# Kernel optimization log

Measured on AMD Instinct MI355X. Metric: run time of the kernel, lower is better.

Reference implementation:

```python
import jax, jax.numpy as jnp
import numpy as np

B, S, D, H = 4, 2048, 1024, 16
DH = D // H  # 64


def setup_inputs() -> dict:
    key = jax.random.key(0)
    ks = jax.random.split(key, 7)
    scale = 1.0 / np.sqrt(DH)
    return {
        "sequences": jax.random.normal(ks[0], (B, S, D), dtype=jnp.float32),
        # torch Linear weights: [out, in] per head -> stacked [H, DH, DH]
        "Wq": jax.random.uniform(ks[1], (H, DH, DH), jnp.float32, -scale, scale),
        "bq": jax.random.uniform(ks[2], (H, DH), jnp.float32, -scale, scale),
        "Wk": jax.random.uniform(ks[3], (H, DH, DH), jnp.float32, -scale, scale),
        "bk": jax.random.uniform(ks[4], (H, DH), jnp.float32, -scale, scale),
        "Wv": jax.random.uniform(ks[5], (H, DH, DH), jnp.float32, -scale, scale),
        "bv": jax.random.uniform(ks[6], (H, DH), jnp.float32, -scale, scale),
    }


def reference(sequences, Wq, bq, Wk, bk, Wv, bv):
    # split d into heads: [B, S, H, DH]
    x = sequences.reshape(B, S, H, DH)
    # per-head Linear: y = x @ W.T + b
    q = jnp.einsum("bshd,hed->bshe", x, Wq) + bq
    k = jnp.einsum("bshd,hed->bshe", x, Wk) + bk
    v = jnp.einsum("bshd,hed->bshe", x, Wv) + bv
    # scaled dot-product attention per head
    scores = jnp.einsum("bshd,bthd->bhst", q, k) / jnp.sqrt(jnp.float32(DH))
    attn = jax.nn.softmax(scores, axis=-1)
    out = jnp.einsum("bhst,bthd->bshd", attn, v)
    # hstack heads back to [B, S, D]
    return out.reshape(B, S, D)
```

## Files before the change

kernel.cpp:

```cpp
#include <hip/hip_runtime.h>
#include <hip/hip_bf16.h>


typedef unsigned short u16;
typedef unsigned int   u32;
typedef float  f32x4   __attribute__((ext_vector_type(4)));
typedef float  f32x16  __attribute__((ext_vector_type(16)));
typedef __bf16 bf16x4  __attribute__((ext_vector_type(4)));
typedef __bf16 bf16x8  __attribute__((ext_vector_type(8)));

#define NB 4
#define SS 2048
#define DDIM 1024
#define NH 16
#define DH 64

static __device__ __forceinline__ float fexp2(float x) {
#if __has_builtin(__builtin_amdgcn_exp2f)
    return __builtin_amdgcn_exp2f(x);
#else
    return exp2f(x);
#endif
}
static __device__ __forceinline__ bf16x4 cvt4(f32x4 v) {
    return __builtin_convertvector(v, bf16x4);
}
static __device__ __forceinline__ bf16x8 cvt8(f32x4 lo, f32x4 hi) {
    return __builtin_shufflevector(cvt4(lo), cvt4(hi), 0, 1, 2, 3, 4, 5, 6, 7);
}

#define WST 72

__global__ __launch_bounds__(256) void qkv_kernel(
        const float* __restrict__ x,
        const float* __restrict__ Wq, const float* __restrict__ bq,
        const float* __restrict__ Wk, const float* __restrict__ bk,
        const float* __restrict__ Wv, const float* __restrict__ bv,
        u16* __restrict__ Qw, u16* __restrict__ Kw, u16* __restrict__ Vt) {
    __shared__ __align__(16) u16 W_lds[3 * DH * WST];

    const int tid  = threadIdx.x;
    const int w    = tid >> 6;
    const int lane = tid & 63;
    const int quad = lane >> 4;
    const int c    = lane & 15;
    const int bid  = blockIdx.x;
    const int bh   = bid & 63;
    const int s0   = (bid >> 6) * 256;
    const int b    = bh >> 4, h = bh & 15;

    {
        const float* Wsrc[3] = {Wq + h*DH*DH, Wk + h*DH*DH, Wv + h*DH*DH};
        #pragma unroll
        for (int j = 0; j < 6; ++j) {
            const int m = j >> 1;
            const int chunk = ((j & 1) << 8) + tid;
            const float* src = Wsrc[m] + chunk * 8;
            f32x4 lo = *(const f32x4*)src;
            f32x4 hi = *(const f32x4*)(src + 4);
            const int row = chunk >> 3, c8 = chunk & 7;
            *(bf16x8*)&W_lds[(m*DH + row) * WST + c8*8] = cvt8(lo, hi);
        }
    }
    __syncthreads();

    bf16x8 wf[3][4][2];
    #pragma unroll
    for (int m = 0; m < 3; ++m)
        #pragma unroll
        for (int mt = 0; mt < 4; ++mt)
            #pragma unroll
            for (int kh = 0; kh < 2; ++kh)
                wf[m][mt][kh] = *(const bf16x8*)&W_lds[(m*DH + mt*16 + c) * WST + kh*32 + quad*8];

    f32x4 biasQK[2][4];
    float biasV[4];
    #pragma unroll
    for (int mt = 0; mt < 4; ++mt) {
        biasQK[0][mt] = *(const f32x4*)(bq + h*DH + mt*16 + quad*4);
        biasQK[1][mt] = *(const f32x4*)(bk + h*DH + mt*16 + quad*4);
        biasV[mt] = bv[h*DH + mt*16 + c];
    }

    const size_t qkbase = (size_t)bh * SS * DH;
    const size_t vtbase = (size_t)bh * DH * SS;

    #pragma unroll 1
    for (int g = 0; g < 4; ++g) {
        const int sb = s0 + w*64 + g*16;
        const float* xr = x + ((size_t)(b * SS + sb + c)) * DDIM + h * DH;
        bf16x8 xb[2];
        #pragma unroll
        for (int kh = 0; kh < 2; ++kh) {
            f32x4 lo = *(const f32x4*)(xr + kh*32 + quad*8);
            f32x4 hi = *(const f32x4*)(xr + kh*32 + quad*8 + 4);
            xb[kh] = cvt8(lo, hi);
        }

        const int srow = sb + c;
        const int tq = srow & 31;
        const int sK = (srow & ~31) | (tq & 3)
                     | (((tq >> 3) & 1) << 2)
                     | (((tq >> 2) & 1) << 3)
                     | (((tq >> 4) & 1) << 4);

        #pragma unroll
        for (int m = 0; m < 2; ++m) {
            const float scale = (m == 0) ? 0.18033688f : 1.0f;
            u16* base = (m == 0 ? Qw : Kw) + qkbase + (size_t)(m == 0 ? srow : sK) * DH;
            #pragma unroll
            for (int mt = 0; mt < 4; ++mt) {
                f32x4 acc = {0.f, 0.f, 0.f, 0.f};
                acc = __builtin_amdgcn_mfma_f32_16x16x32_bf16(wf[m][mt][0], xb[0], acc, 0, 0, 0);
                acc = __builtin_amdgcn_mfma_f32_16x16x32_bf16(wf[m][mt][1], xb[1], acc, 0, 0, 0);
                f32x4 v = (acc + biasQK[m][mt]) * scale;
                *(bf16x4*)(base + mt*16 + quad*4) = cvt4(v);
            }
        }
        #pragma unroll
        for (int nt = 0; nt < 4; ++nt) {
            f32x4 acc = {0.f, 0.f, 0.f, 0.f};
            acc = __builtin_amdgcn_mfma_f32_16x16x32_bf16(xb[0], wf[2][nt][0], acc, 0, 0, 0);
            acc = __builtin_amdgcn_mfma_f32_16x16x32_bf16(xb[1], wf[2][nt][1], acc, 0, 0, 0);
            f32x4 v = acc + biasV[nt];
            u16* dst = Vt + vtbase + (size_t)(nt*16 + c) * SS + sb + quad*4;
            *(bf16x4*)dst = cvt4(v);
        }
    }
}

#define KT 64
#define KST 72
#define VST 72

#define Z16 {0.f,0.f,0.f,0.f,0.f,0.f,0.f,0.f,0.f,0.f,0.f,0.f,0.f,0.f,0.f,0.f}

#define GROUP(g) do {                                                          \
        bf16x8 ka0 = *(const bf16x8*)&Kl[((g)*32 + l31) * KST +  0 + hi*8];    \
        bf16x8 ka1 = *(const bf16x8*)&Kl[((g)*32 + l31) * KST + 16 + hi*8];    \
        bf16x8 ka2 = *(const bf16x8*)&Kl[((g)*32 + l31) * KST + 32 + hi*8];    \
        bf16x8 ka3 = *(const bf16x8*)&Kl[((g)*32 + l31) * KST + 48 + hi*8];    \
        bf16x8 vf00 = *(const bf16x8*)&Vl[( 0 + l31) * VST + (g)*32 +  0 + hi*8]; \
        bf16x8 vf01 = *(const bf16x8*)&Vl[( 0 + l31) * VST + (g)*32 + 16 + hi*8]; \
        bf16x8 vf10 = *(const bf16x8*)&Vl[(32 + l31) * VST + (g)*32 +  0 + hi*8]; \
        bf16x8 vf11 = *(const bf16x8*)&Vl[(32 + l31) * VST + (g)*32 + 16 + hi*8]; \
        __builtin_amdgcn_s_setprio(1);                                         \
        f32x16 s = Z16;                                                        \
        s = __builtin_amdgcn_mfma_f32_32x32x16_bf16(ka0, qf[0], s, 0,0,0);     \
        s = __builtin_amdgcn_mfma_f32_32x32x16_bf16(ka1, qf[1], s, 0,0,0);     \
        s = __builtin_amdgcn_mfma_f32_32x32x16_bf16(ka2, qf[2], s, 0,0,0);     \
        s = __builtin_amdgcn_mfma_f32_32x32x16_bf16(ka3, qf[3], s, 0,0,0);     \
        _Pragma("unroll")                                                      \
        for (int r = 0; r < 16; ++r) s[r] = fexp2(s[r]);                       \
        lp += (((s[0]+s[1])+(s[2]+s[3])) + ((s[4]+s[5])+(s[6]+s[7])))          \
            + (((s[8]+s[9])+(s[10]+s[11])) + ((s[12]+s[13])+(s[14]+s[15])));   \
        bf16x8 pf0 = cvt8((f32x4){s[0],s[1],s[2],s[3]},                        \
                          (f32x4){s[4],s[5],s[6],s[7]});                       \
        bf16x8 pf1 = cvt8((f32x4){s[8],s[9],s[10],s[11]},                      \
                          (f32x4){s[12],s[13],s[14],s[15]});                   \
        o0 = __builtin_amdgcn_mfma_f32_32x32x16_bf16(vf00, pf0, o0, 0,0,0);    \
        o0 = __builtin_amdgcn_mfma_f32_32x32x16_bf16(vf01, pf1, o0, 0,0,0);    \
        o1 = __builtin_amdgcn_mfma_f32_32x32x16_bf16(vf10, pf0, o1, 0,0,0);    \
        o1 = __builtin_amdgcn_mfma_f32_32x32x16_bf16(vf11, pf1, o1, 0,0,0);    \
        __builtin_amdgcn_s_setprio(0);                                         \
    } while (0)

__global__ __launch_bounds__(256, 2) void attn_kernel(
        const u16* __restrict__ Qw, const u16* __restrict__ Kw,
        const u16* __restrict__ Vt, float* __restrict__ out) {
    __shared__ __align__(16) u16 K_lds[2][KT * KST];
    __shared__ __align__(16) u16 V_lds[2][DH * VST];

    const int tid  = threadIdx.x;
    const int w    = tid >> 6;
    const int lane = tid & 63;
    const int l31  = lane & 31;
    const int hi   = lane >> 5;
    const int bid  = blockIdx.x;
    const int bh   = bid & 63;
    const int q0   = (bid >> 6) * 128;
    const int qw   = q0 + w * 32;

    const u16* Qb = Qw + (size_t)bh * SS * DH;
    const u16* Kb = Kw + (size_t)bh * SS * DH;
    const u16* Vb = Vt + (size_t)bh * DH * SS;

    bf16x8 qf[4];
    {
        const u16* qrow = Qb + (size_t)(qw + l31) * DH;
        #pragma unroll
        for (int m = 0; m < 4; ++m)
            qf[m] = *(const bf16x8*)(qrow + m*16 + hi*8);
    }

    f32x16 o0 = Z16, o1 = Z16;
    float lp = 0.f;

    const int strow = tid >> 2;
    const int stcol = (tid & 3) * 16;
    const int kofs  = strow * KST + stcol;
    const int vofs  = strow * VST + stcol;

    uint4 kr0 = *(const uint4*)(Kb + (size_t)strow * DH + stcol);
    uint4 kr1 = *(const uint4*)(Kb + (size_t)strow * DH + stcol + 8);
    uint4 vr0 = *(const uint4*)(Vb + (size_t)strow * SS + stcol);
    uint4 vr1 = *(const uint4*)(Vb + (size_t)strow * SS + stcol + 8);

    #pragma unroll 1
    for (int t0 = 0; t0 < SS; t0 += KT) {
        const int bsel = (t0 >> 6) & 1;
        u16* Kl = K_lds[bsel];
        u16* Vl = V_lds[bsel];
        *(uint4*)&Kl[kofs]     = kr0;
        *(uint4*)&Kl[kofs + 8] = kr1;
        *(uint4*)&Vl[vofs]     = vr0;
        *(uint4*)&Vl[vofs + 8] = vr1;
        __syncthreads();
        int tn = t0 + KT; if (tn >= SS) tn = 0;
        kr0 = *(const uint4*)(Kb + (size_t)(tn + strow) * DH + stcol);
        kr1 = *(const uint4*)(Kb + (size_t)(tn + strow) * DH + stcol + 8);
        vr0 = *(const uint4*)(Vb + (size_t)strow * SS + tn + stcol);
        vr1 = *(const uint4*)(Vb + (size_t)strow * SS + tn + stcol + 8);

        GROUP(0);
        GROUP(1);
    }

    const int b = bh >> 4, h = bh & 15;
    const float lw = lp + __shfl_xor(lp, 32, 64);
    const float inv = 1.0f / lw;
    const int token = qw + l31;
    float* orow = out + ((size_t)b * SS + token) * DDIM + h * DH;
    #pragma unroll
    for (int rq = 0; rq < 4; ++rq) {
        f32x4 v0 = {o0[4*rq+0], o0[4*rq+1], o0[4*rq+2], o0[4*rq+3]};
        f32x4 v1 = {o1[4*rq+0], o1[4*rq+1], o1[4*rq+2], o1[4*rq+3]};
        v0 = v0 * inv;
        v1 = v1 * inv;
        *(f32x4*)(orow +      8*rq + 4*hi) = v0;
        *(f32x4*)(orow + 32 + 8*rq + 4*hi) = v1;
    }
}

extern "C" void kernel_launch(void* const* d_in, const int* in_sizes, int n_in,
                              void* d_out, int out_size, void* d_ws, size_t ws_size,
                              hipStream_t stream) {
    const float* x  = (const float*)d_in[0];
    const float* Wq = (const float*)d_in[1];
    const float* bq = (const float*)d_in[2];
    const float* Wk = (const float*)d_in[3];
    const float* bk = (const float*)d_in[4];
    const float* Wv = (const float*)d_in[5];
    const float* bv = (const float*)d_in[6];

    u16* Qw = (u16*)d_ws;
    u16* Kw = Qw + (size_t)NB * NH * SS * DH;
    u16* Vt = Kw + (size_t)NB * NH * SS * DH;

    qkv_kernel<<<64 * (SS / 256), 256, 0, stream>>>(
        x, Wq, bq, Wk, bk, Wv, bv, Qw, Kw, Vt);
    attn_kernel<<<64 * (SS / 128), 256, 0, stream>>>(Qw, Kw, Vt, (float*)d_out);
}
```

Baseline: 186.0 us.

## Software-pipeline QK^T of the next group with exp/PV of the previous

```diff
diff --git a/kernel.cpp b/kernel.cpp
--- a/kernel.cpp
+++ b/kernel.cpp
@@ -135,21 +135,26 @@
 
 #define Z16 {0.f,0.f,0.f,0.f,0.f,0.f,0.f,0.f,0.f,0.f,0.f,0.f,0.f,0.f,0.f,0.f}
 
-#define GROUP(g) do {                                                          \
-        bf16x8 ka0 = *(const bf16x8*)&Kl[((g)*32 + l31) * KST +  0 + hi*8];    \
-        bf16x8 ka1 = *(const bf16x8*)&Kl[((g)*32 + l31) * KST + 16 + hi*8];    \
-        bf16x8 ka2 = *(const bf16x8*)&Kl[((g)*32 + l31) * KST + 32 + hi*8];    \
-        bf16x8 ka3 = *(const bf16x8*)&Kl[((g)*32 + l31) * KST + 48 + hi*8];    \
-        bf16x8 vf00 = *(const bf16x8*)&Vl[( 0 + l31) * VST + (g)*32 +  0 + hi*8]; \
-        bf16x8 vf01 = *(const bf16x8*)&Vl[( 0 + l31) * VST + (g)*32 + 16 + hi*8]; \
-        bf16x8 vf10 = *(const bf16x8*)&Vl[(32 + l31) * VST + (g)*32 +  0 + hi*8]; \
-        bf16x8 vf11 = *(const bf16x8*)&Vl[(32 + l31) * VST + (g)*32 + 16 + hi*8]; \
-        __builtin_amdgcn_s_setprio(1);                                         \
-        f32x16 s = Z16;                                                        \
-        s = __builtin_amdgcn_mfma_f32_32x32x16_bf16(ka0, qf[0], s, 0,0,0);     \
-        s = __builtin_amdgcn_mfma_f32_32x32x16_bf16(ka1, qf[1], s, 0,0,0);     \
-        s = __builtin_amdgcn_mfma_f32_32x32x16_bf16(ka2, qf[2], s, 0,0,0);     \
-        s = __builtin_amdgcn_mfma_f32_32x32x16_bf16(ka3, qf[3], s, 0,0,0);     \
+#define QKG(Kp, g, sdst) do {                                                  \
+        bf16x8 ka0 = *(const bf16x8*)&Kp[((g)*32 + l31) * KST +  0 + hi*8];    \
+        bf16x8 ka1 = *(const bf16x8*)&Kp[((g)*32 + l31) * KST + 16 + hi*8];    \
+        bf16x8 ka2 = *(const bf16x8*)&Kp[((g)*32 + l31) * KST + 32 + hi*8];    \
+        bf16x8 ka3 = *(const bf16x8*)&Kp[((g)*32 + l31) * KST + 48 + hi*8];    \
+        sdst = (f32x16)Z16;                                                    \
+        sdst = __builtin_amdgcn_mfma_f32_32x32x16_bf16(ka0, qf[0], sdst, 0,0,0); \
+        sdst = __builtin_amdgcn_mfma_f32_32x32x16_bf16(ka1, qf[1], sdst, 0,0,0); \
+        sdst = __builtin_amdgcn_mfma_f32_32x32x16_bf16(ka2, qf[2], sdst, 0,0,0); \
+        sdst = __builtin_amdgcn_mfma_f32_32x32x16_bf16(ka3, qf[3], sdst, 0,0,0); \
+    } while (0)
+
+#define VFR(Vp, g, vf) do {                                                    \
+        vf[0] = *(const bf16x8*)&Vp[( 0 + l31) * VST + (g)*32 +  0 + hi*8];    \
+        vf[1] = *(const bf16x8*)&Vp[( 0 + l31) * VST + (g)*32 + 16 + hi*8];    \
+        vf[2] = *(const bf16x8*)&Vp[(32 + l31) * VST + (g)*32 +  0 + hi*8];    \
+        vf[3] = *(const bf16x8*)&Vp[(32 + l31) * VST + (g)*32 + 16 + hi*8];    \
+    } while (0)
+
+#define FIN(s, vf) do {                                                        \
         _Pragma("unroll")                                                      \
         for (int r = 0; r < 16; ++r) s[r] = fexp2(s[r]);                       \
         lp += (((s[0]+s[1])+(s[2]+s[3])) + ((s[4]+s[5])+(s[6]+s[7])))          \
@@ -158,11 +163,10 @@
                           (f32x4){s[4],s[5],s[6],s[7]});                       \
         bf16x8 pf1 = cvt8((f32x4){s[8],s[9],s[10],s[11]},                      \
                           (f32x4){s[12],s[13],s[14],s[15]});                   \
-        o0 = __builtin_amdgcn_mfma_f32_32x32x16_bf16(vf00, pf0, o0, 0,0,0);    \
-        o0 = __builtin_amdgcn_mfma_f32_32x32x16_bf16(vf01, pf1, o0, 0,0,0);    \
-        o1 = __builtin_amdgcn_mfma_f32_32x32x16_bf16(vf10, pf0, o1, 0,0,0);    \
-        o1 = __builtin_amdgcn_mfma_f32_32x32x16_bf16(vf11, pf1, o1, 0,0,0);    \
-        __builtin_amdgcn_s_setprio(0);                                         \
+        o0 = __builtin_amdgcn_mfma_f32_32x32x16_bf16(vf[0], pf0, o0, 0,0,0);   \
+        o0 = __builtin_amdgcn_mfma_f32_32x32x16_bf16(vf[1], pf1, o0, 0,0,0);   \
+        o1 = __builtin_amdgcn_mfma_f32_32x32x16_bf16(vf[2], pf0, o1, 0,0,0);   \
+        o1 = __builtin_amdgcn_mfma_f32_32x32x16_bf16(vf[3], pf1, o1, 0,0,0);   \
     } while (0)
 
 __global__ __launch_bounds__(256, 2) void attn_kernel(
@@ -206,24 +210,56 @@
     uint4 vr0 = *(const uint4*)(Vb + (size_t)strow * SS + stcol);
     uint4 vr1 = *(const uint4*)(Vb + (size_t)strow * SS + stcol + 8);
 
+    *(uint4*)&K_lds[0][kofs]     = kr0;
+    *(uint4*)&K_lds[0][kofs + 8] = kr1;
+    *(uint4*)&V_lds[0][vofs]     = vr0;
+    *(uint4*)&V_lds[0][vofs + 8] = vr1;
+    __syncthreads();
+    kr0 = *(const uint4*)(Kb + (size_t)(KT + strow) * DH + stcol);
+    kr1 = *(const uint4*)(Kb + (size_t)(KT + strow) * DH + stcol + 8);
+    vr0 = *(const uint4*)(Vb + (size_t)strow * SS + KT + stcol);
+    vr1 = *(const uint4*)(Vb + (size_t)strow * SS + KT + stcol + 8);
+
+    f32x16 sP, sN;
+    bf16x8 vfP[4], vfN[4];
+    QKG(K_lds[0], 0, sP);
+    VFR(V_lds[0], 0, vfP);
+
     #pragma unroll 1
-    for (int t0 = 0; t0 < SS; t0 += KT) {
-        const int bsel = (t0 >> 6) & 1;
-        u16* Kl = K_lds[bsel];
-        u16* Vl = V_lds[bsel];
-        *(uint4*)&Kl[kofs]     = kr0;
-        *(uint4*)&Kl[kofs + 8] = kr1;
-        *(uint4*)&Vl[vofs]     = vr0;
-        *(uint4*)&Vl[vofs + 8] = vr1;
+    for (int t = 0; t < 31; ++t) {
+        const int cb = t & 1;
+        u16* Klc = K_lds[cb];
+        u16* Vlc = V_lds[cb];
+        u16* Kln = K_lds[cb ^ 1];
+        u16* Vln = V_lds[cb ^ 1];
+
+        QKG(Klc, 1, sN);
+        VFR(Vlc, 1, vfN);
+        FIN(sP, vfP);
+
+        *(uint4*)&Kln[kofs]     = kr0;
+        *(uint4*)&Kln[kofs + 8] = kr1;
+        *(uint4*)&Vln[vofs]     = vr0;
+        *(uint4*)&Vln[vofs + 8] = vr1;
         __syncthreads();
-        int tn = t0 + KT; if (tn >= SS) tn = 0;
+        int tn = (t + 2) * KT; if (tn >= SS) tn = 0;
         kr0 = *(const uint4*)(Kb + (size_t)(tn + strow) * DH + stcol);
         kr1 = *(const uint4*)(Kb + (size_t)(tn + strow) * DH + stcol + 8);
         vr0 = *(const uint4*)(Vb + (size_t)strow * SS + tn + stcol);
         vr1 = *(const uint4*)(Vb + (size_t)strow * SS + tn + stcol + 8);
 
-        GROUP(0);
-        GROUP(1);
+        QKG(Kln, 0, sP);
+        VFR(Vln, 0, vfP);
+        FIN(sN, vfN);
+    }
+
+    {
+        u16* Klc = K_lds[1];
+        u16* Vlc = V_lds[1];
+        QKG(Klc, 1, sN);
+        VFR(Vlc, 1, vfN);
+        FIN(sP, vfP);
+        FIN(sN, vfN);
     }
 
     const int b = bh >> 4, h = bh & 15;
```

After: 188.8 us. Within noise of the previous version (+1.5%).
